# Optimization experiments

Measured on AMD Instinct MI355X. Metric: run time of the kernel, lower is better.

## Reference

```python
import jax, jax.numpy as jnp
import numpy as np

IN_SIZE = 1024
HIDDEN = 50
OUT_DIM = 8
BATCH = 16384
BN_EPS = 1e-5


def _gf(h, W1, b1, W2, b2):
    # graph_fusion: Linear -> LeakyReLU(0.2) -> Linear -> Tanh
    t = h @ W1 + b1
    t = jnp.where(t > 0, t, 0.2 * t)
    return jnp.tanh(t @ W2 + b2)


def _lrelu(z):
    return jnp.where(z > 0, z, 0.01 * z)  # F.leaky_relu default slope


def _dot(p, q):
    return jnp.sum(p * q, axis=-1)  # batched [B,1,D]@[B,D,1] -> [B]


def setup_inputs() -> dict:
    key = jax.random.key(0)
    ks = jax.random.split(key, 16)
    d, h, o = IN_SIZE, HIDDEN, OUT_DIM
    s = lambda n: 1.0 / np.sqrt(n)
    return {
        "x": jax.random.normal(ks[0], (BATCH, 3, d), jnp.float32),
        "att_W": jax.random.normal(ks[1], (d, 1), jnp.float32) * s(d),
        "att_b": jnp.zeros((1,), jnp.float32),
        "gf_W1": jax.random.normal(ks[2], (2 * d, 64), jnp.float32) * s(2 * d),
        "gf_b1": jnp.zeros((64,), jnp.float32),
        "gf_W2": jax.random.normal(ks[3], (64, d), jnp.float32) * s(64),
        "gf_b2": jnp.zeros((d,), jnp.float32),
        "bn_gamma": jnp.ones((3 * d,), jnp.float32),
        "bn_beta": jnp.zeros((3 * d,), jnp.float32),
        "l1_W": jax.random.normal(ks[4], (3 * d, h), jnp.float32) * s(3 * d),
        "l1_b": jnp.zeros((h,), jnp.float32),
        "l2_W": jax.random.normal(ks[5], (h, h), jnp.float32) * s(h),
        "l2_b": jnp.zeros((h,), jnp.float32),
        "l3_W": jax.random.normal(ks[6], (h, o), jnp.float32) * s(h),
        "l3_b": jnp.zeros((o,), jnp.float32),
    }


def _forward(x, att_W, att_b, gf_W1, gf_b1, gf_W2, gf_b2,
             bn_gamma, bn_beta, l1_W, l1_b, l2_W, l2_b, l3_W, l3_b):
    a1, v1, l1_ = x[:, 0, :], x[:, 1, :], x[:, 2, :]
    gf = lambda p, q: _gf(jnp.concatenate([p, q], axis=1), gf_W1, gf_b1, gf_W2, gf_b2)

    # unimodal attention weights, softmax over the 3 modalities
    att = jnp.tanh(x @ att_W + att_b)[..., 0]          # [B,3]
    w_uni = jax.nn.softmax(att, axis=1)                # [B,3]
    sa, sv, sl = w_uni[:, 0], w_uni[:, 1], w_uni[:, 2]
    unimodal = (sa[:, None] * a1 + sv[:, None] * v1 + sl[:, None] * l1_) / 3.0

    a = jax.nn.softmax(a1, axis=1)
    v = jax.nn.softmax(v1, axis=1)
    l = jax.nn.softmax(l1_, axis=1)
    sav = (sa + sv) / (_dot(a, v) + 0.5)
    sal = (sa + sl) / (_dot(a, l) + 0.5)
    svl = (sl + sv) / (_dot(v, l) + 0.5)
    w_bi = jax.nn.softmax(jnp.stack([sav, sal, svl], axis=1), axis=1)  # [B,3]

    a_v = _lrelu(w_bi[:, 0:1] * gf(a1, v1))
    a_l = _lrelu(w_bi[:, 1:2] * gf(a1, l1_))
    v_l = _lrelu(w_bi[:, 2:3] * gf(v1, l1_))
    bimodal = (a_v + a_l + v_l) / 3.0

    a_v2 = jax.nn.softmax(a_v, axis=1)
    a_l2 = jax.nn.softmax(a_l, axis=1)
    v_l2 = jax.nn.softmax(v_l, axis=1)
    savvl = (sav + svl) / (_dot(a_v2, v_l2) + 0.5)
    saavl = (sav + sal) / (_dot(a_v2, a_l2) + 0.5)
    savll = (sal + svl) / (_dot(a_l2, v_l2) + 0.5)
    savl = (sav + sl) / (_dot(a_v2, l) + 0.5)
    salv = (sal + sv) / (_dot(a_l2, v) + 0.5)
    svla = (sa + svl) / (_dot(v_l2, a) + 0.5)
    w_tri = jax.nn.softmax(
        jnp.stack([savvl, saavl, savll, savl, salv, svla], axis=1), axis=1)  # [B,6]

    avvl = _lrelu(w_tri[:, 0:1] * gf(a_v, v_l))
    aavl = _lrelu(w_tri[:, 1:2] * gf(a_v, a_l))
    avll = _lrelu(w_tri[:, 2:3] * gf(v_l, a_l))
    avl = _lrelu(w_tri[:, 3:4] * gf(a_v, l1_))
    alv = _lrelu(w_tri[:, 4:5] * gf(a_l, v1))
    vla = _lrelu(w_tri[:, 5:6] * gf(v_l, a1))
    trimodal = (avvl + aavl + avll + avl + alv + vla) / 6.0

    fusion = jnp.concatenate([unimodal, bimodal, trimodal], axis=1)  # [B,3*in]
    # BatchNorm1d in eval mode: running_mean=0, running_var=1
    fusion = fusion * (bn_gamma / jnp.sqrt(1.0 + BN_EPS)) + bn_beta
    y = jnp.tanh(fusion @ l1_W + l1_b)
    y = jnp.tanh(y @ l2_W + l2_b)
    y2 = jax.nn.softmax(y @ l3_W + l3_b, axis=1)
    total_weights = jnp.concatenate([w_uni, w_bi, w_tri], axis=1)  # [B,12]
    return y2, total_weights


def reference(x, att_W, att_b, gf_W1, gf_b1, gf_W2, gf_b2,
              bn_gamma, bn_beta, l1_W, l1_b, l2_W, l2_b, l3_W, l3_b):
    return _forward(x, att_W, att_b, gf_W1, gf_b1, gf_W2, gf_b2,
                    bn_gamma, bn_beta, l1_W, l1_b, l2_W, l2_b, l3_W, l3_b)
```

## Files before the change

### kernel.cpp

```cpp
#include <hip/hip_runtime.h>
#include <math.h>

#define NB 16384
#define DD 1024
#define KF 5120

typedef unsigned short u16;
typedef unsigned int u32;
typedef __attribute__((ext_vector_type(8))) short bf16x8;
typedef __attribute__((ext_vector_type(4))) float f32x4;

__device__ __forceinline__ float bf2f(u16 u){
  return __uint_as_float(((unsigned)u) << 16);
}
__device__ __forceinline__ u16 f2bf(float f){
  unsigned u = __float_as_uint(f);
  return (u16)((u + 0x7fffu + ((u >> 16) & 1u)) >> 16);
}
__device__ __forceinline__ u16 f2bf_tr(float f){
  return (u16)(__float_as_uint(f) >> 16);
}
__device__ __forceinline__ u32 pack2bf(float a, float b){
  return (u32)f2bf(a) | ((u32)f2bf(b) << 16);
}
__device__ __forceinline__ float fast_tanh(float x){
  float e = __expf(2.0f * x);
  return 1.0f - 2.0f * __builtin_amdgcn_rcpf(e + 1.0f);
}
__device__ __forceinline__ float wredsum(float x){
  #pragma unroll
  for(int o = 32; o >= 1; o >>= 1) x += __shfl_xor(x, o);
  return x;
}
__device__ __forceinline__ float wredmax(float x){
  #pragma unroll
  for(int o = 32; o >= 1; o >>= 1) x = fmaxf(x, __shfl_xor(x, o));
  return x;
}
__device__ __forceinline__ void gll16(const void* g, void* l){
  __builtin_amdgcn_global_load_lds(
      (const __attribute__((address_space(1))) u32*)g,
      (__attribute__((address_space(3))) u32*)l, 16, 0, 0);
}

__global__ __launch_bounds__(256) void kpre(
    const float* __restrict__ W1, const float* __restrict__ W2,
    const float* __restrict__ gamma, const float* __restrict__ beta,
    const float* __restrict__ l1W, const float* __restrict__ l1b,
    u16* __restrict__ Wb1, u16* __restrict__ W2T, u16* __restrict__ WpT,
    float* __restrict__ bp)
{
  __shared__ float red[4][64];
  int b = blockIdx.x, tid = threadIdx.x;
  if(b < 512){
    int idx = b*256 + tid;
    int n = idx >> 10, k = idx & 1023;
    float v = (n < 64) ? W1[(size_t)k*64 + n] : W1[(size_t)(1024+k)*64 + (n-64)];
    Wb1[idx] = f2bf(v);
  } else if(b < 768){
    int idx = (b-512)*256 + tid;
    int c = idx >> 6, k = idx & 63;
    W2T[idx] = f2bf(W2[(size_t)k*DD + c]);
  } else if(b < 2048){
    int idx = (b-768)*256 + tid;
    int j = idx / KF, kk = idx - j*KF;
    const float gsc = 1.0f / sqrtf(1.0f + 1e-5f);
    int korig; float sc;
    if(kk < 1024){ korig = kk; sc = 1.f; }
    else if(kk < 4096){ korig = 1024 + ((kk - 1024) & 1023); sc = 1.0f/3.0f; }
    else { korig = 2048 + (kk - 4096); sc = 1.f; }
    float v = (j < 50) ? l1W[(size_t)korig*50 + j] * gamma[korig] * gsc * sc : 0.f;
    WpT[(size_t)j*KF + kk] = f2bf(v);
  } else {
    int j = tid & 63, seg = tid >> 6;
    float s = 0.f;
    if(j < 50){
      for(int k = seg*768; k < seg*768 + 768; k++)
        s = fmaf(beta[k], l1W[(size_t)k*50 + j], s);
    }
    red[seg][j] = s;
    __syncthreads();
    if(seg == 0){
      float t = red[0][j] + red[1][j] + red[2][j] + red[3][j];
      bp[j] = (j < 50) ? (l1b[j] + t) : 0.f;
    }
  }
}

__global__ __launch_bounds__(256) void k1_stats(
    const float* __restrict__ x, const float* __restrict__ attW,
    const float* __restrict__ attb, float* __restrict__ stats,
    u16* __restrict__ uniB, u16* __restrict__ xb, float* __restrict__ tw)
{
  int wave = threadIdx.x >> 6, lane = threadIdx.x & 63;
  int r = blockIdx.x * 4 + wave;
  const float2* xr  = (const float2*)(x + (size_t)r * 3 * DD);
  const float2* aw2 = (const float2*)attW;
  float2 a[8], v[8], l[8];
  float dA=0.f,dV=0.f,dL=0.f, mA=-1e30f,mV=-1e30f,mL=-1e30f;
  #pragma unroll
  for(int i = 0; i < 8; i++){
    int k2 = lane + i*64;
    a[i] = xr[k2]; v[i] = xr[512+k2]; l[i] = xr[1024+k2];
    float2 w = aw2[k2];
    dA = fmaf(a[i].x, w.x, fmaf(a[i].y, w.y, dA));
    dV = fmaf(v[i].x, w.x, fmaf(v[i].y, w.y, dV));
    dL = fmaf(l[i].x, w.x, fmaf(l[i].y, w.y, dL));
    mA = fmaxf(mA, fmaxf(a[i].x, a[i].y));
    mV = fmaxf(mV, fmaxf(v[i].x, v[i].y));
    mL = fmaxf(mL, fmaxf(l[i].x, l[i].y));
  }
  dA = wredsum(dA); dV = wredsum(dV); dL = wredsum(dL);
  mA = wredmax(mA); mV = wredmax(mV); mL = wredmax(mL);

  u32* xbw = (u32*)(xb + (size_t)3*r*DD);
  #pragma unroll
  for(int i = 0; i < 8; i++){
    int k2 = lane + i*64;
    xbw[k2]      = pack2bf(a[i].x, a[i].y);
    xbw[512+k2]  = pack2bf(v[i].x, v[i].y);
    xbw[1024+k2] = pack2bf(l[i].x, l[i].y);
  }

  float Sa=0.f,Sv=0.f,Sl=0.f,Eav=0.f,Eal=0.f,Evl=0.f;
  #pragma unroll
  for(int i = 0; i < 8; i++){
    float eax = __expf(a[i].x-mA), eay = __expf(a[i].y-mA);
    float evx = __expf(v[i].x-mV), evy = __expf(v[i].y-mV);
    float elx = __expf(l[i].x-mL), ely = __expf(l[i].y-mL);
    Sa += eax+eay; Sv += evx+evy; Sl += elx+ely;
    Eav += eax*evx + eay*evy; Eal += eax*elx + eay*ely; Evl += evx*elx + evy*ely;
  }
  Sa = wredsum(Sa); Sv = wredsum(Sv); Sl = wredsum(Sl);
  Eav = wredsum(Eav); Eal = wredsum(Eal); Evl = wredsum(Evl);

  float ab = attb[0];
  float ta = fast_tanh(dA + ab), tv = fast_tanh(dV + ab), tl = fast_tanh(dL + ab);
  float mm = fmaxf(ta, fmaxf(tv, tl));
  float e0 = __expf(ta-mm), e1 = __expf(tv-mm), e2 = __expf(tl-mm);
  float ss = e0 + e1 + e2;
  float sa = e0/ss, sv = e1/ss, sl = e2/ss;
  float dav = Eav/(Sa*Sv), dal = Eal/(Sa*Sl), dvl = Evl/(Sv*Sl);
  float sav = (sa+sv)/(dav+0.5f);
  float sal = (sa+sl)/(dal+0.5f);
  float svl = (sv+sl)/(dvl+0.5f);
  float m2 = fmaxf(sav, fmaxf(sal, svl));
  float f0 = __expf(sav-m2), f1 = __expf(sal-m2), f2 = __expf(svl-m2);
  float s2 = f0 + f1 + f2;
  float wb0 = f0/s2, wb1 = f1/s2, wb2 = f2/s2;

  if(lane == 0){
    float* st = stats + (size_t)r*24;
    st[0]=sa; st[1]=sv; st[2]=sl;
    st[3]=wb0; st[4]=wb1; st[5]=wb2;
    st[6]=sav; st[7]=sal; st[8]=svl;
    st[9]=mA; st[10]=Sa; st[11]=mV; st[12]=Sv; st[13]=mL; st[14]=Sl;
    float* twr = tw + (size_t)r*12;
    twr[0]=sa; twr[1]=sv; twr[2]=sl; twr[3]=wb0; twr[4]=wb1; twr[5]=wb2;
  }
  u32* uniw = (u32*)(uniB + (size_t)r*DD);
  #pragma unroll
  for(int i = 0; i < 8; i++){
    int k2 = lane + i*64;
    float ux = (sa*a[i].x + sv*v[i].x + sl*l[i].x) * (1.0f/3.0f);
    float uy = (sa*a[i].y + sv*v[i].y + sl*l[i].y) * (1.0f/3.0f);
    uniw[k2] = pack2bf(ux, uy);
  }
}

__global__ __launch_bounds__(256) void kg1v3(
    const u16* __restrict__ src, const u16* __restrict__ Wb1,
    float* __restrict__ UV)
{
  __shared__ u16 Asm[2][64*64];
  int tid = threadIdx.x;
  int wv = tid >> 6, lane = tid & 63;
  int fr = lane & 15, kg = lane >> 4;
  int mb = blockIdx.x * 64;

  int r8 = lane >> 3, p = lane & 7;
  int sp = p ^ r8;
  int m0 = mb + (2*wv)*8 + r8;
  int m1 = mb + (2*wv+1)*8 + r8;
  const u16* gsrc0 = src + (size_t)m0*1024 + sp*8;
  const u16* gsrc1 = src + (size_t)m1*1024 + sp*8;

  f32x4 acc[4][2];
  #pragma unroll
  for(int rf = 0; rf < 4; rf++)
    #pragma unroll
    for(int nf = 0; nf < 2; nf++) acc[rf][nf] = (f32x4){0.f,0.f,0.f,0.f};

  gll16(gsrc0, &Asm[0][(2*wv)*512]);
  gll16(gsrc1, &Asm[0][(2*wv+1)*512]);
  __syncthreads();

  int buf = 0;
  for(int ci = 0; ci < 16; ci++){
    int k0 = ci*64;
    if(ci < 15){
      gll16(gsrc0 + k0 + 64, &Asm[buf^1][(2*wv)*512]);
      gll16(gsrc1 + k0 + 64, &Asm[buf^1][(2*wv+1)*512]);
    }
    #pragma unroll
    for(int ks = 0; ks < 2; ks++){
      bf16x8 a[4];
      #pragma unroll
      for(int rf = 0; rf < 4; rf++){
        int row = rf*16 + fr;
        int slot = (ks*4 + kg) ^ (row & 7);
        a[rf] = *(const bf16x8*)&Asm[buf][row*64 + slot*8];
      }
      #pragma unroll
      for(int nf = 0; nf < 2; nf++){
        int col = wv*32 + nf*16 + fr;
        bf16x8 b = *(const bf16x8*)&Wb1[(size_t)col*1024 + k0 + ks*32 + kg*8];
        #pragma unroll
        for(int rf = 0; rf < 4; rf++)
          acc[rf][nf] = __builtin_amdgcn_mfma_f32_16x16x32_bf16(a[rf], b, acc[rf][nf], 0, 0, 0);
      }
    }
    __syncthreads();
    buf ^= 1;
  }

  #pragma unroll
  for(int rf = 0; rf < 4; rf++)
    #pragma unroll
    for(int nf = 0; nf < 2; nf++)
      #pragma unroll
      for(int q = 0; q < 4; q++)
        UV[(size_t)(mb + rf*16 + kg*4 + q)*128 + wv*32 + nf*16 + fr] = acc[rf][nf][q];
}

__global__ __launch_bounds__(256) void kBI(
    const float* __restrict__ UV1, const u16* __restrict__ xb,
    const u16* __restrict__ W2T, const u16* __restrict__ Wb1,
    const u16* __restrict__ WpT, const float* __restrict__ b1,
    const float* __restrict__ b2, float* __restrict__ stats,
    float* __restrict__ tw, float* __restrict__ UV2, float* __restrict__ y1g)
{
  __shared__ u16 Tsm[3][16][64];
  __shared__ u16 Osm[4][16][264];
  __shared__ float stro[16][15];
  int tid = threadIdx.x;
  int wv = tid >> 6, lane = tid & 63;
  int fr = lane & 15, kg = lane >> 4;
  int Rb = blockIdx.x * 16;

  if(tid < 240){
    int r = tid / 15, c = tid - r*15;
    stro[r][c] = stats[(size_t)(Rb + r)*24 + c];
  }
  for(int i = tid; i < 384; i += 256){
    int g = i & 7, r = (i >> 3) & 15, p = i >> 7;
    int R = Rb + r;
    int up = (p == 2) ? 1 : 0;
    int vp = (p == 0) ? 1 : 2;
    const float* Up = UV1 + (size_t)(3*R + up)*128 + g*8;
    const float* Vp = UV1 + (size_t)(3*R + vp)*128 + 64 + g*8;
    float4 u0 = *(const float4*)Up, u1 = *(const float4*)(Up+4);
    float4 v0 = *(const float4*)Vp, v1 = *(const float4*)(Vp+4);
    float4 bb0 = *(const float4*)(b1 + g*8), bb1 = *(const float4*)(b1 + g*8 + 4);
    float t[8] = {u0.x+v0.x+bb0.x, u0.y+v0.y+bb0.y, u0.z+v0.z+bb0.z, u0.w+v0.w+bb0.w,
                  u1.x+v1.x+bb1.x, u1.y+v1.y+bb1.y, u1.z+v1.z+bb1.z, u1.w+v1.w+bb1.w};
    bf16x8 o;
    #pragma unroll
    for(int j = 0; j < 8; j++){
      float tv = t[j] > 0.f ? t[j] : 0.2f*t[j];
      o[j] = (short)f2bf_tr(tv);
    }
    *(bf16x8*)&Tsm[p][r][(g ^ (r & 7))*8] = o;
  }
  __syncthreads();

  f32x4 acc_uv[3][2];
  #pragma unroll
  for(int p = 0; p < 3; p++){ acc_uv[p][0] = (f32x4){0,0,0,0}; acc_uv[p][1] = (f32x4){0,0,0,0}; }
  f32x4 accy = (f32x4){0,0,0,0};
  int srow = tid >> 4, sc0 = (tid & 15) * 16;
  float SP[9] = {0,0,0,0,0,0,0,0,0};
  float mAr = stro[srow][9],  Sar = stro[srow][10];
  float mVr = stro[srow][11], Svr = stro[srow][12];
  float mLr = stro[srow][13], Slr = stro[srow][14];
  size_t xbase = (size_t)3*(Rb + srow)*DD;

  for(int cg = 0; cg < 4; cg++){
    f32x4 acc[3][4];
    #pragma unroll
    for(int p = 0; p < 3; p++)
      #pragma unroll
      for(int cf = 0; cf < 4; cf++) acc[p][cf] = (f32x4){0,0,0,0};
    #pragma unroll
    for(int ks = 0; ks < 2; ks++){
      bf16x8 a[3];
      #pragma unroll
      for(int p = 0; p < 3; p++)
        a[p] = *(const bf16x8*)&Tsm[p][fr][(((ks<<2)+kg) ^ (fr & 7))*8];
      #pragma unroll
      for(int cf = 0; cf < 4; cf++){
        bf16x8 b = *(const bf16x8*)&W2T[(size_t)(cg*256 + wv*64 + cf*16 + fr)*64
                                        + ks*32 + kg*8];
        #pragma unroll
        for(int p = 0; p < 3; p++)
          acc[p][cf] = __builtin_amdgcn_mfma_f32_16x16x32_bf16(a[p], b, acc[p][cf], 0, 0, 0);
      }
    }
    __syncthreads();
    #pragma unroll
    for(int q = 0; q < 4; q++){
      int row = kg*4 + q;
      #pragma unroll
      for(int cf = 0; cf < 4; cf++){
        int cloc = wv*64 + cf*16 + fr;
        float b2c = b2[cg*256 + cloc];
        float sm = 0.f;
        #pragma unroll
        for(int p = 0; p < 3; p++){
          float g = stro[row][3+p] * fast_tanh(acc[p][cf][q] + b2c);
          float val = g > 0.f ? g : 0.01f*g;
          Osm[p][row][cloc] = f2bf(val);
          sm += val;
        }
        Osm[3][row][cloc] = f2bf_tr(sm);
      }
    }
    __syncthreads();

    {
      const u32* xa1 = (const u32*)(xb + xbase + cg*256 + sc0);
      const u32* xv1 = (const u32*)(xb + xbase + DD + cg*256 + sc0);
      const u32* xl1 = (const u32*)(xb + xbase + 2*DD + cg*256 + sc0);
      #pragma unroll
      for(int j = 0; j < 8; j++){
        u32 oav = *(const u32*)&Osm[0][srow][sc0 + 2*j];
        u32 oal = *(const u32*)&Osm[1][srow][sc0 + 2*j];
        u32 ovl = *(const u32*)&Osm[2][srow][sc0 + 2*j];
        u32 wa = xa1[j], wvv = xv1[j], wl = xl1[j];
        float eavx = __expf(bf2f((u16)oav)), eavy = __expf(bf2f((u16)(oav>>16)));
        float ealx = __expf(bf2f((u16)oal)), ealy = __expf(bf2f((u16)(oal>>16)));
        float evlx = __expf(bf2f((u16)ovl)), evly = __expf(bf2f((u16)(ovl>>16)));
        float eax = __expf(bf2f((u16)wa)-mAr),  eay = __expf(bf2f((u16)(wa>>16))-mAr);
        float evx = __expf(bf2f((u16)wvv)-mVr), evy = __expf(bf2f((u16)(wvv>>16))-mVr);
        float elx = __expf(bf2f((u16)wl)-mLr),  ely = __expf(bf2f((u16)(wl>>16))-mLr);
        SP[0] += eavx+eavy; SP[1] += ealx+ealy; SP[2] += evlx+evly;
        SP[3] += eavx*evlx + eavy*evly;
        SP[4] += eavx*ealx + eavy*ealy;
        SP[5] += ealx*evlx + ealy*evly;
        SP[6] += eavx*elx + eavy*ely;
        SP[7] += ealx*evx + ealy*evy;
        SP[8] += evlx*eax + evly*eay;
      }
    }
    #pragma unroll
    for(int ks8 = 0; ks8 < 8; ks8++){
      bf16x8 a[3];
      #pragma unroll
      for(int p = 0; p < 3; p++)
        a[p] = *(const bf16x8*)&Osm[p][fr][ks8*32 + kg*8];
      #pragma unroll
      for(int nf = 0; nf < 2; nf++){
        int n = wv*32 + nf*16 + fr;
        bf16x8 b = *(const bf16x8*)&Wb1[(size_t)n*1024 + cg*256 + ks8*32 + kg*8];
        #pragma unroll
        for(int p = 0; p < 3; p++)
          acc_uv[p][nf] = __builtin_amdgcn_mfma_f32_16x16x32_bf16(a[p], b, acc_uv[p][nf], 0, 0, 0);
      }
    }
    #pragma unroll
    for(int kq = 0; kq < 4; kq++)
      #pragma unroll
      for(int ks = 0; ks < 2; ks++){
        bf16x8 a = *(const bf16x8*)&Osm[3][fr][kq*64 + ks*32 + kg*8];
        bf16x8 b = *(const bf16x8*)&WpT[(size_t)(wv*16 + fr)*KF + 1024 + cg*256
                                        + kq*64 + ks*32 + kg*8];
        accy = __builtin_amdgcn_mfma_f32_16x16x32_bf16(a, b, accy, 0, 0, 0);
      }
  }

  #pragma unroll
  for(int p = 0; p < 3; p++)
    #pragma unroll
    for(int nf = 0; nf < 2; nf++)
      #pragma unroll
      for(int q = 0; q < 4; q++)
        UV2[(size_t)(3*(Rb + kg*4 + q) + p)*128 + wv*32 + nf*16 + fr] = acc_uv[p][nf][q];
  #pragma unroll
  for(int q = 0; q < 4; q++)
    y1g[(size_t)(Rb + kg*4 + q)*64 + wv*16 + fr] = accy[q];

  #pragma unroll
  for(int s = 0; s < 9; s++){
    SP[s] += __shfl_xor(SP[s], 1);
    SP[s] += __shfl_xor(SP[s], 2);
    SP[s] += __shfl_xor(SP[s], 4);
    SP[s] += __shfl_xor(SP[s], 8);
  }
  if((tid & 15) == 0){
    int r = srow;
    float sa=stro[r][0], sv=stro[r][1], sl=stro[r][2];
    float sav=stro[r][6], sal=stro[r][7], svl=stro[r][8];
    float d1 = SP[3]/(SP[0]*SP[2]), d2 = SP[4]/(SP[0]*SP[1]), d3 = SP[5]/(SP[1]*SP[2]);
    float d4 = SP[6]/(SP[0]*Slr),   d5 = SP[7]/(SP[1]*Svr),   d6 = SP[8]/(SP[2]*Sar);
    float t0 = (sav+svl)/(d1+0.5f);
    float t1 = (sav+sal)/(d2+0.5f);
    float t2 = (sal+svl)/(d3+0.5f);
    float t3 = (sav+sl)/(d4+0.5f);
    float t4 = (sal+sv)/(d5+0.5f);
    float t5 = (sa+svl)/(d6+0.5f);
    float mx = fmaxf(fmaxf(fmaxf(t0,t1),fmaxf(t2,t3)),fmaxf(t4,t5));
    float g0=__expf(t0-mx),g1=__expf(t1-mx),g2=__expf(t2-mx);
    float g3=__expf(t3-mx),g4=__expf(t4-mx),g5=__expf(t5-mx);
    float gs = g0+g1+g2+g3+g4+g5;
    float wt[6] = {g0/gs,g1/gs,g2/gs,g3/gs,g4/gs,g5/gs};
    float* st = stats + (size_t)(Rb + r)*24;
    float* twr = tw + (size_t)(Rb + r)*12;
    #pragma unroll
    for(int p = 0; p < 6; p++){ st[15+p] = wt[p]; twr[6+p] = wt[p]; }
  }
}

__global__ __launch_bounds__(256) void kTRI(
    const float* __restrict__ UV2, const float* __restrict__ UV1,
    const u16* __restrict__ W2T, const u16* __restrict__ WpT,
    const float* __restrict__ b1, const float* __restrict__ b2,
    const float* __restrict__ stats, float* __restrict__ y1g)
{
  __shared__ u16 Tsm[6][16][64];
  __shared__ u16 Osm[16][264];
  __shared__ float stw[16][6];
  int tid = threadIdx.x;
  int wv = tid >> 6, lane = tid & 63;
  int fr = lane & 15, kg = lane >> 4;
  int Rb = blockIdx.x * 16;

  if(tid < 96){
    int r = tid / 6, p = tid - r*6;
    stw[r][p] = stats[(size_t)(Rb + r)*24 + 15 + p];
  }
  for(int i = tid; i < 768; i += 256){
    int g = i & 7, r = (i >> 3) & 15, p = i >> 7;
    int R = Rb + r;
    int up = (0x210200 >> (p*4)) & 15;
    int vp = (0x012112 >> (p*4)) & 15;
    const float* VB = (p < 3) ? UV2 : UV1;
    const float* Up = UV2 + (size_t)(3*R + up)*128 + g*8;
    const float* Vp = VB  + (size_t)(3*R + vp)*128 + 64 + g*8;
    float4 u0 = *(const float4*)Up, u1 = *(const float4*)(Up+4);
    float4 v0 = *(const float4*)Vp, v1 = *(const float4*)(Vp+4);
    float4 bb0 = *(const float4*)(b1 + g*8), bb1 = *(const float4*)(b1 + g*8 + 4);
    float t[8] = {u0.x+v0.x+bb0.x, u0.y+v0.y+bb0.y, u0.z+v0.z+bb0.z, u0.w+v0.w+bb0.w,
                  u1.x+v1.x+bb1.x, u1.y+v1.y+bb1.y, u1.z+v1.z+bb1.z, u1.w+v1.w+bb1.w};
    bf16x8 o;
    #pragma unroll
    for(int j = 0; j < 8; j++){
      float tv = t[j] > 0.f ? t[j] : 0.2f*t[j];
      o[j] = (short)f2bf_tr(tv);
    }
    *(bf16x8*)&Tsm[p][r][(g ^ (r & 7))*8] = o;
  }
  __syncthreads();

  f32x4 accy = (f32x4){0,0,0,0};
  for(int cg = 0; cg < 4; cg++){
    f32x4 acc[6][4];
    #pragma unroll
    for(int p = 0; p < 6; p++)
      #pragma unroll
      for(int cf = 0; cf < 4; cf++) acc[p][cf] = (f32x4){0,0,0,0};
    #pragma unroll
    for(int ks = 0; ks < 2; ks++){
      bf16x8 a[6];
      #pragma unroll
      for(int p = 0; p < 6; p++)
        a[p] = *(const bf16x8*)&Tsm[p][fr][(((ks<<2)+kg) ^ (fr & 7))*8];
      #pragma unroll
      for(int cf = 0; cf < 4; cf++){
        bf16x8 b = *(const bf16x8*)&W2T[(size_t)(cg*256 + wv*64 + cf*16 + fr)*64
                                        + ks*32 + kg*8];
        #pragma unroll
        for(int p = 0; p < 6; p++)
          acc[p][cf] = __builtin_amdgcn_mfma_f32_16x16x32_bf16(a[p], b, acc[p][cf], 0, 0, 0);
      }
    }
    __syncthreads();
    #pragma unroll
    for(int q = 0; q < 4; q++){
      int row = kg*4 + q;
      #pragma unroll
      for(int cf = 0; cf < 4; cf++){
        int cloc = wv*64 + cf*16 + fr;
        float b2c = b2[cg*256 + cloc];
        float s = 0.f;
        #pragma unroll
        for(int p = 0; p < 6; p++){
          float g = stw[row][p] * fast_tanh(acc[p][cf][q] + b2c);
          s += g > 0.f ? g : 0.01f*g;
        }
        Osm[row][cloc] = f2bf_tr(s * (1.0f/6.0f));
      }
    }
    __syncthreads();
    #pragma unroll
    for(int kq = 0; kq < 4; kq++)
      #pragma unroll
      for(int ks = 0; ks < 2; ks++){
        bf16x8 a = *(const bf16x8*)&Osm[fr][kq*64 + ks*32 + kg*8];
        bf16x8 b = *(const bf16x8*)&WpT[(size_t)(wv*16 + fr)*KF + 4096 + cg*256
                                        + kq*64 + ks*32 + kg*8];
        accy = __builtin_amdgcn_mfma_f32_16x16x32_bf16(a, b, accy, 0, 0, 0);
      }
  }
  #pragma unroll
  for(int q = 0; q < 4; q++){
    size_t idx = (size_t)(Rb + kg*4 + q)*64 + wv*16 + fr;
    y1g[idx] += accy[q];
  }
}

__global__ __launch_bounds__(256) void k6v5(
    const u16* __restrict__ uniB, const u16* __restrict__ WpT,
    const float* __restrict__ y1g, const float* __restrict__ bp,
    const float* __restrict__ l2W, const float* __restrict__ l2b,
    const float* __restrict__ l3W, const float* __restrict__ l3b,
    float* __restrict__ y2out)
{
  __shared__ __align__(16) char smem[37952];
  u16*  Asm = (u16*)smem;
  float* W2s = (float*)(smem + 16384);
  float* W3s = (float*)(smem + 16384 + 12800);
  float* Ys  = (float*)smem;
  float* Ys2 = (float*)(smem + 16384 + 12800 + 1600);

  int tid = threadIdx.x;
  int wv = tid >> 6, lane = tid & 63;
  int fr = lane & 15, kg = lane >> 4;
  int rb = blockIdx.x * 32;

  for(int t = tid; t < 3200; t += 256){
    int c = t & 63;
    W2s[t] = (c < 50) ? l2W[(t >> 6)*50 + c] : 0.f;
  }
  for(int t = tid; t < 400; t += 256) W3s[t] = l3W[t];

  int r8 = lane >> 3, pp = lane & 7;
  int sp = pp ^ r8;
  const u16* gsrc = uniB + (size_t)(rb + wv*8 + r8)*DD + sp*8;
  const u16* bptr = WpT  + (size_t)(wv*16 + fr)*KF + kg*8;

  f32x4 acc[2];
  acc[0] = (f32x4){0.f,0.f,0.f,0.f};
  acc[1] = (f32x4){0.f,0.f,0.f,0.f};

  gll16(gsrc,      &Asm[wv*1024]);
  gll16(gsrc + 64, &Asm[wv*1024 + 512]);
  __syncthreads();

  int buf = 0;
  for(int ci = 0; ci < 8; ci++){
    int k0 = ci*128;
    if(ci < 7){
      gll16(gsrc + k0 + 128, &Asm[(buf^1)*4096 + wv*1024]);
      gll16(gsrc + k0 + 192, &Asm[(buf^1)*4096 + wv*1024 + 512]);
    }
    #pragma unroll
    for(int kh = 0; kh < 2; kh++){
      #pragma unroll
      for(int ks = 0; ks < 2; ks++){
        bf16x8 b = *(const bf16x8*)(bptr + k0 + kh*64 + ks*32);
        #pragma unroll
        for(int rf = 0; rf < 2; rf++){
          int row = rf*16 + fr;
          int slot = ((ks<<2) + kg) ^ (row & 7);
          bf16x8 a = *(const bf16x8*)&Asm[buf*4096 + (row>>3)*1024 + kh*512
                                          + (row & 7)*64 + slot*8];
          acc[rf] = __builtin_amdgcn_mfma_f32_16x16x32_bf16(a, b, acc[rf], 0, 0, 0);
        }
      }
    }
    __syncthreads();
    buf ^= 1;
  }

  {
    int col = wv*16 + fr;
    float bpc = bp[col];
    #pragma unroll
    for(int rf = 0; rf < 2; rf++)
      #pragma unroll
      for(int q = 0; q < 4; q++){
        int row = rf*16 + kg*4 + q;
        if(col < 50){
          float z = acc[rf][q] + y1g[(size_t)(rb + row)*64 + col] + bpc;
          Ys[row*56 + col] = fast_tanh(z);
        }
      }
  }
  __syncthreads();

  {
    int r = tid >> 3, cg = (tid & 7) * 7;
    float a2[7] = {0,0,0,0,0,0,0};
    for(int k = 0; k < 50; k++){
      float yv = Ys[r*56 + k];
      #pragma unroll
      for(int c = 0; c < 7; c++) a2[c] = fmaf(yv, W2s[k*64 + cg + c], a2[c]);
    }
    #pragma unroll
    for(int c = 0; c < 7; c++){
      int cc = cg + c;
      if(cc < 50) Ys2[r*56 + cc] = fast_tanh(a2[c] + l2b[cc]);
    }
  }
  __syncthreads();

  {
    int r = tid >> 3, c = tid & 7;
    float z = l3b[c];
    for(int k = 0; k < 50; k++) z = fmaf(Ys2[r*56 + k], W3s[k*8 + c], z);
    float m = z;
    m = fmaxf(m, __shfl_xor(m, 1));
    m = fmaxf(m, __shfl_xor(m, 2));
    m = fmaxf(m, __shfl_xor(m, 4));
    float e = __expf(z - m);
    float s = e;
    s += __shfl_xor(s, 1); s += __shfl_xor(s, 2); s += __shfl_xor(s, 4);
    y2out[(size_t)(rb + r)*8 + c] = e / s;
  }
}

extern "C" void kernel_launch(void* const* d_in, const int* in_sizes, int n_in,
                              void* d_out, int out_size, void* d_ws, size_t ws_size,
                              hipStream_t stream)
{
  (void)in_sizes; (void)n_in; (void)out_size; (void)ws_size;
  const float* x    = (const float*)d_in[0];
  const float* attW = (const float*)d_in[1];
  const float* attb = (const float*)d_in[2];
  const float* gfW1 = (const float*)d_in[3];
  const float* gfb1 = (const float*)d_in[4];
  const float* gfW2 = (const float*)d_in[5];
  const float* gfb2 = (const float*)d_in[6];
  const float* bng  = (const float*)d_in[7];
  const float* bnb  = (const float*)d_in[8];
  const float* l1W  = (const float*)d_in[9];
  const float* l1b  = (const float*)d_in[10];
  const float* l2W  = (const float*)d_in[11];
  const float* l2b  = (const float*)d_in[12];
  const float* l3W  = (const float*)d_in[13];
  const float* l3b  = (const float*)d_in[14];

  float* out = (float*)d_out;
  float* tw  = out + (size_t)NB*8;

  float* ws    = (float*)d_ws;
  float* stats = ws;
  float* UV1   = stats + (size_t)NB*24;
  float* UV2   = UV1 + (size_t)3*NB*128;
  float* bp    = UV2 + (size_t)3*NB*128;
  float* y1g   = bp + 64;
  u16* WpT     = (u16*)(y1g + (size_t)NB*64);
  u16* Wb1     = WpT + (size_t)64*KF;
  u16* W2T     = Wb1 + (size_t)128*1024;
  u16* xb      = W2T + (size_t)1024*64;
  u16* uniB    = xb + (size_t)3*NB*DD;

  kpre<<<dim3(2049), dim3(256), 0, stream>>>(gfW1, gfW2, bng, bnb, l1W, l1b,
                                             Wb1, W2T, WpT, bp);
  k1_stats<<<dim3(NB/4), dim3(256), 0, stream>>>(x, attW, attb, stats, uniB, xb, tw);
  kg1v3<<<dim3(3*NB/64), dim3(256), 0, stream>>>(xb, Wb1, UV1);
  kBI<<<dim3(NB/16), dim3(256), 0, stream>>>(UV1, xb, W2T, Wb1, WpT,
                                             gfb1, gfb2, stats, tw, UV2, y1g);
  kTRI<<<dim3(NB/16), dim3(256), 0, stream>>>(UV2, UV1, W2T, WpT,
                                              gfb1, gfb2, stats, y1g);
  k6v5<<<dim3(NB/32), dim3(256), 0, stream>>>(uniB, WpT, y1g, bp,
                                              l2W, l2b, l3W, l3b, out);
}
```

Measured before the change: 449.9 us.

## Split bimodal/trimodal stages across column slabs with atomics and separate GEMM pass

The bimodal and trimodal kernels now run on a 2D grid with one block per (16-row group, 256-column slab) instead of looping over four column groups serially. Partial y1 contributions and softmax statistics are accumulated with atomicAdd into buffers that the prep kernel zeroes. The bimodal outputs are written to a bf16 Fcat buffer, and a templated reuse of the first-layer GEMM kernel computes UV2 from it instead of fusing that GEMM into the bimodal kernel. k1_stats also moves to float4 loads and uint2 stores. This raises parallelism and occupancy, at the cost of extra global traffic for Fcat, an additional kernel launch and atomic contention.

After: 379.9 us. 1.18x faster.

```diff
diff --git a/kernel.cpp b/kernel.cpp
--- a/kernel.cpp
+++ b/kernel.cpp
@@ -48,7 +48,7 @@
     const float* __restrict__ gamma, const float* __restrict__ beta,
     const float* __restrict__ l1W, const float* __restrict__ l1b,
     u16* __restrict__ Wb1, u16* __restrict__ W2T, u16* __restrict__ WpT,
-    float* __restrict__ bp)
+    float* __restrict__ bp, float* __restrict__ y1g, float* __restrict__ spart)
 {
   __shared__ float red[4][64];
   int b = blockIdx.x, tid = threadIdx.x;
@@ -71,6 +71,12 @@
     else { korig = 2048 + (kk - 4096); sc = 1.f; }
     float v = (j < 50) ? l1W[(size_t)korig*50 + j] * gamma[korig] * gsc * sc : 0.f;
     WpT[(size_t)j*KF + kk] = f2bf(v);
+  } else if(b < 3072){
+    int idx = (b - 2048)*256 + tid;
+    ((float4*)y1g)[idx] = make_float4(0.f,0.f,0.f,0.f);
+  } else if(b < 3216){
+    int idx = (b - 3072)*256 + tid;
+    ((float4*)spart)[idx] = make_float4(0.f,0.f,0.f,0.f);
   } else {
     int j = tid & 63, seg = tid >> 6;
     float s = 0.f;
@@ -94,42 +100,44 @@
 {
   int wave = threadIdx.x >> 6, lane = threadIdx.x & 63;
   int r = blockIdx.x * 4 + wave;
-  const float2* xr  = (const float2*)(x + (size_t)r * 3 * DD);
-  const float2* aw2 = (const float2*)attW;
-  float2 a[8], v[8], l[8];
+  const float4* xr  = (const float4*)(x + (size_t)r * 3 * DD);
+  const float4* aw4 = (const float4*)attW;
+  float4 a[4], v[4], l[4];
   float dA=0.f,dV=0.f,dL=0.f, mA=-1e30f,mV=-1e30f,mL=-1e30f;
   #pragma unroll
-  for(int i = 0; i < 8; i++){
-    int k2 = lane + i*64;
-    a[i] = xr[k2]; v[i] = xr[512+k2]; l[i] = xr[1024+k2];
-    float2 w = aw2[k2];
-    dA = fmaf(a[i].x, w.x, fmaf(a[i].y, w.y, dA));
-    dV = fmaf(v[i].x, w.x, fmaf(v[i].y, w.y, dV));
-    dL = fmaf(l[i].x, w.x, fmaf(l[i].y, w.y, dL));
-    mA = fmaxf(mA, fmaxf(a[i].x, a[i].y));
-    mV = fmaxf(mV, fmaxf(v[i].x, v[i].y));
-    mL = fmaxf(mL, fmaxf(l[i].x, l[i].y));
+  for(int i = 0; i < 4; i++){
+    int k4 = lane + i*64;
+    a[i] = xr[k4]; v[i] = xr[256+k4]; l[i] = xr[512+k4];
+    float4 w = aw4[k4];
+    dA = fmaf(a[i].x,w.x, fmaf(a[i].y,w.y, fmaf(a[i].z,w.z, fmaf(a[i].w,w.w, dA))));
+    dV = fmaf(v[i].x,w.x, fmaf(v[i].y,w.y, fmaf(v[i].z,w.z, fmaf(v[i].w,w.w, dV))));
+    dL = fmaf(l[i].x,w.x, fmaf(l[i].y,w.y, fmaf(l[i].z,w.z, fmaf(l[i].w,w.w, dL))));
+    mA = fmaxf(mA, fmaxf(fmaxf(a[i].x,a[i].y), fmaxf(a[i].z,a[i].w)));
+    mV = fmaxf(mV, fmaxf(fmaxf(v[i].x,v[i].y), fmaxf(v[i].z,v[i].w)));
+    mL = fmaxf(mL, fmaxf(fmaxf(l[i].x,l[i].y), fmaxf(l[i].z,l[i].w)));
   }
   dA = wredsum(dA); dV = wredsum(dV); dL = wredsum(dL);
   mA = wredmax(mA); mV = wredmax(mV); mL = wredmax(mL);
 
-  u32* xbw = (u32*)(xb + (size_t)3*r*DD);
-  #pragma unroll
-  for(int i = 0; i < 8; i++){
-    int k2 = lane + i*64;
-    xbw[k2]      = pack2bf(a[i].x, a[i].y);
-    xbw[512+k2]  = pack2bf(v[i].x, v[i].y);
-    xbw[1024+k2] = pack2bf(l[i].x, l[i].y);
+  uint2* xbw = (uint2*)(xb + (size_t)3*r*DD);
+  #pragma unroll
+  for(int i = 0; i < 4; i++){
+    int k4 = lane + i*64;
+    xbw[k4]     = make_uint2(pack2bf(a[i].x,a[i].y), pack2bf(a[i].z,a[i].w));
+    xbw[256+k4] = make_uint2(pack2bf(v[i].x,v[i].y), pack2bf(v[i].z,v[i].w));
+    xbw[512+k4] = make_uint2(pack2bf(l[i].x,l[i].y), pack2bf(l[i].z,l[i].w));
   }
 
   float Sa=0.f,Sv=0.f,Sl=0.f,Eav=0.f,Eal=0.f,Evl=0.f;
   #pragma unroll
-  for(int i = 0; i < 8; i++){
-    float eax = __expf(a[i].x-mA), eay = __expf(a[i].y-mA);
-    float evx = __expf(v[i].x-mV), evy = __expf(v[i].y-mV);
-    float elx = __expf(l[i].x-mL), ely = __expf(l[i].y-mL);
-    Sa += eax+eay; Sv += evx+evy; Sl += elx+ely;
-    Eav += eax*evx + eay*evy; Eal += eax*elx + eay*ely; Evl += evx*elx + evy*ely;
+  for(int i = 0; i < 4; i++){
+    float ea0=__expf(a[i].x-mA), ea1=__expf(a[i].y-mA), ea2=__expf(a[i].z-mA), ea3=__expf(a[i].w-mA);
+    float ev0=__expf(v[i].x-mV), ev1=__expf(v[i].y-mV), ev2=__expf(v[i].z-mV), ev3=__expf(v[i].w-mV);
+    float el0=__expf(l[i].x-mL), el1=__expf(l[i].y-mL), el2=__expf(l[i].z-mL), el3=__expf(l[i].w-mL);
+    Sa += ea0+ea1+ea2+ea3; Sv += ev0+ev1+ev2+ev3; Sl += el0+el1+el2+el3;
+    Eav += ea0*ev0 + ea1*ev1 + ea2*ev2 + ea3*ev3;
+    Eal += ea0*el0 + ea1*el1 + ea2*el2 + ea3*el3;
+    Evl += ev0*el0 + ev1*el1 + ev2*el2 + ev3*el3;
   }
   Sa = wredsum(Sa); Sv = wredsum(Sv); Sl = wredsum(Sl);
   Eav = wredsum(Eav); Eal = wredsum(Eal); Evl = wredsum(Evl);
@@ -158,16 +166,19 @@
     float* twr = tw + (size_t)r*12;
     twr[0]=sa; twr[1]=sv; twr[2]=sl; twr[3]=wb0; twr[4]=wb1; twr[5]=wb2;
   }
-  u32* uniw = (u32*)(uniB + (size_t)r*DD);
-  #pragma unroll
-  for(int i = 0; i < 8; i++){
-    int k2 = lane + i*64;
-    float ux = (sa*a[i].x + sv*v[i].x + sl*l[i].x) * (1.0f/3.0f);
-    float uy = (sa*a[i].y + sv*v[i].y + sl*l[i].y) * (1.0f/3.0f);
-    uniw[k2] = pack2bf(ux, uy);
-  }
-}
-
+  uint2* uniw = (uint2*)(uniB + (size_t)r*DD);
+  #pragma unroll
+  for(int i = 0; i < 4; i++){
+    int k4 = lane + i*64;
+    float u0 = (sa*a[i].x + sv*v[i].x + sl*l[i].x) * (1.0f/3.0f);
+    float u1 = (sa*a[i].y + sv*v[i].y + sl*l[i].y) * (1.0f/3.0f);
+    float u2 = (sa*a[i].z + sv*v[i].z + sl*l[i].z) * (1.0f/3.0f);
+    float u3 = (sa*a[i].w + sv*v[i].w + sl*l[i].w) * (1.0f/3.0f);
+    uniw[k4] = make_uint2(pack2bf(u0,u1), pack2bf(u2,u3));
+  }
+}
+
+template<int FCAT>
 __global__ __launch_bounds__(256) void kg1v3(
     const u16* __restrict__ src, const u16* __restrict__ Wb1,
     float* __restrict__ UV)
@@ -182,8 +193,17 @@
   int sp = p ^ r8;
   int m0 = mb + (2*wv)*8 + r8;
   int m1 = mb + (2*wv+1)*8 + r8;
-  const u16* gsrc0 = src + (size_t)m0*1024 + sp*8;
-  const u16* gsrc1 = src + (size_t)m1*1024 + sp*8;
+  size_t b0, b1;
+  if(FCAT){
+    int R0 = m0/3, R1 = m1/3;
+    b0 = (size_t)R0*KF + (size_t)(1 + (m0 - 3*R0))*1024;
+    b1 = (size_t)R1*KF + (size_t)(1 + (m1 - 3*R1))*1024;
+  } else {
+    b0 = (size_t)m0*1024;
+    b1 = (size_t)m1*1024;
+  }
+  const u16* gsrc0 = src + b0 + sp*8;
+  const u16* gsrc1 = src + b1 + sp*8;
 
   f32x4 acc[4][2];
   #pragma unroll
@@ -233,12 +253,12 @@
         UV[(size_t)(mb + rf*16 + kg*4 + q)*128 + wv*32 + nf*16 + fr] = acc[rf][nf][q];
 }
 
-__global__ __launch_bounds__(256) void kBI(
+__global__ __launch_bounds__(256) void kL2bi(
     const float* __restrict__ UV1, const u16* __restrict__ xb,
-    const u16* __restrict__ W2T, const u16* __restrict__ Wb1,
-    const u16* __restrict__ WpT, const float* __restrict__ b1,
-    const float* __restrict__ b2, float* __restrict__ stats,
-    float* __restrict__ tw, float* __restrict__ UV2, float* __restrict__ y1g)
+    const u16* __restrict__ W2T, const u16* __restrict__ WpT,
+    const float* __restrict__ b1, const float* __restrict__ b2,
+    const float* __restrict__ stats, u16* __restrict__ Fcat,
+    float* __restrict__ y1g, float* __restrict__ spart)
 {
   __shared__ u16 Tsm[3][16][64];
   __shared__ u16 Osm[4][16][264];
@@ -247,10 +267,11 @@
   int wv = tid >> 6, lane = tid & 63;
   int fr = lane & 15, kg = lane >> 4;
   int Rb = blockIdx.x * 16;
+  int slab = blockIdx.y;
 
   if(tid < 240){
-    int r = tid / 15, c = tid - r*15;
-    stro[r][c] = stats[(size_t)(Rb + r)*24 + c];
+    int rr = tid / 15, c = tid - rr*15;
+    stro[rr][c] = stats[(size_t)(Rb + rr)*24 + c];
   }
   for(int i = tid; i < 384; i += 256){
     int g = i & 7, r = (i >> 3) & 15, p = i >> 7;
@@ -274,134 +295,144 @@
   }
   __syncthreads();
 
-  f32x4 acc_uv[3][2];
-  #pragma unroll
-  for(int p = 0; p < 3; p++){ acc_uv[p][0] = (f32x4){0,0,0,0}; acc_uv[p][1] = (f32x4){0,0,0,0}; }
-  f32x4 accy = (f32x4){0,0,0,0};
-  int srow = tid >> 4, sc0 = (tid & 15) * 16;
-  float SP[9] = {0,0,0,0,0,0,0,0,0};
-  float mAr = stro[srow][9],  Sar = stro[srow][10];
-  float mVr = stro[srow][11], Svr = stro[srow][12];
-  float mLr = stro[srow][13], Slr = stro[srow][14];
-  size_t xbase = (size_t)3*(Rb + srow)*DD;
-
-  for(int cg = 0; cg < 4; cg++){
-    f32x4 acc[3][4];
+  f32x4 acc[3][4];
+  #pragma unroll
+  for(int p = 0; p < 3; p++)
+    #pragma unroll
+    for(int cf = 0; cf < 4; cf++) acc[p][cf] = (f32x4){0,0,0,0};
+  #pragma unroll
+  for(int ks = 0; ks < 2; ks++){
+    bf16x8 a[3];
     #pragma unroll
     for(int p = 0; p < 3; p++)
-      #pragma unroll
-      for(int cf = 0; cf < 4; cf++) acc[p][cf] = (f32x4){0,0,0,0};
-    #pragma unroll
-    for(int ks = 0; ks < 2; ks++){
-      bf16x8 a[3];
+      a[p] = *(const bf16x8*)&Tsm[p][fr][(((ks<<2)+kg) ^ (fr & 7))*8];
+    #pragma unroll
+    for(int cf = 0; cf < 4; cf++){
+      bf16x8 b = *(const bf16x8*)&W2T[(size_t)(slab*256 + wv*64 + cf*16 + fr)*64
+                                      + ks*32 + kg*8];
       #pragma unroll
       for(int p = 0; p < 3; p++)
-        a[p] = *(const bf16x8*)&Tsm[p][fr][(((ks<<2)+kg) ^ (fr & 7))*8];
-      #pragma unroll
-      for(int cf = 0; cf < 4; cf++){
-        bf16x8 b = *(const bf16x8*)&W2T[(size_t)(cg*256 + wv*64 + cf*16 + fr)*64
-                                        + ks*32 + kg*8];
-        #pragma unroll
-        for(int p = 0; p < 3; p++)
-          acc[p][cf] = __builtin_amdgcn_mfma_f32_16x16x32_bf16(a[p], b, acc[p][cf], 0, 0, 0);
-      }
-    }
-    __syncthreads();
-    #pragma unroll
-    for(int q = 0; q < 4; q++){
-      int row = kg*4 + q;
-      #pragma unroll
-      for(int cf = 0; cf < 4; cf++){
-        int cloc = wv*64 + cf*16 + fr;
-        float b2c = b2[cg*256 + cloc];
-        float sm = 0.f;
-        #pragma unroll
-        for(int p = 0; p < 3; p++){
-          float g = stro[row][3+p] * fast_tanh(acc[p][cf][q] + b2c);
-          float val = g > 0.f ? g : 0.01f*g;
-          Osm[p][row][cloc] = f2bf(val);
-          sm += val;
-        }
-        Osm[3][row][cloc] = f2bf_tr(sm);
-      }
-    }
-    __syncthreads();
-
-    {
-      const u32* xa1 = (const u32*)(xb + xbase + cg*256 + sc0);
-      const u32* xv1 = (const u32*)(xb + xbase + DD + cg*256 + sc0);
-      const u32* xl1 = (const u32*)(xb + xbase + 2*DD + cg*256 + sc0);
-      #pragma unroll
-      for(int j = 0; j < 8; j++){
-        u32 oav = *(const u32*)&Osm[0][srow][sc0 + 2*j];
-        u32 oal = *(const u32*)&Osm[1][srow][sc0 + 2*j];
-        u32 ovl = *(const u32*)&Osm[2][srow][sc0 + 2*j];
-        u32 wa = xa1[j], wvv = xv1[j], wl = xl1[j];
-        float eavx = __expf(bf2f((u16)oav)), eavy = __expf(bf2f((u16)(oav>>16)));
-        float ealx = __expf(bf2f((u16)oal)), ealy = __expf(bf2f((u16)(oal>>16)));
-        float evlx = __expf(bf2f((u16)ovl)), evly = __expf(bf2f((u16)(ovl>>16)));
-        float eax = __expf(bf2f((u16)wa)-mAr),  eay = __expf(bf2f((u16)(wa>>16))-mAr);
-        float evx = __expf(bf2f((u16)wvv)-mVr), evy = __expf(bf2f((u16)(wvv>>16))-mVr);
-        float elx = __expf(bf2f((u16)wl)-mLr),  ely = __expf(bf2f((u16)(wl>>16))-mLr);
-        SP[0] += eavx+eavy; SP[1] += ealx+ealy; SP[2] += evlx+evly;
-        SP[3] += eavx*evlx + eavy*evly;
-        SP[4] += eavx*ealx + eavy*ealy;
-        SP[5] += ealx*evlx + ealy*evly;
-        SP[6] += eavx*elx + eavy*ely;
-        SP[7] += ealx*evx + ealy*evy;
-        SP[8] += evlx*eax + evly*eay;
-      }
-    }
-    #pragma unroll
-    for(int ks8 = 0; ks8 < 8; ks8++){
-      bf16x8 a[3];
-      #pragma unroll
-      for(int p = 0; p < 3; p++)
-        a[p] = *(const bf16x8*)&Osm[p][fr][ks8*32 + kg*8];
-      #pragma unroll
-      for(int nf = 0; nf < 2; nf++){
-        int n = wv*32 + nf*16 + fr;
-        bf16x8 b = *(const bf16x8*)&Wb1[(size_t)n*1024 + cg*256 + ks8*32 + kg*8];
-        #pragma unroll
-        for(int p = 0; p < 3; p++)
-          acc_uv[p][nf] = __builtin_amdgcn_mfma_f32_16x16x32_bf16(a[p], b, acc_uv[p][nf], 0, 0, 0);
-      }
-    }
+        acc[p][cf] = __builtin_amdgcn_mfma_f32_16x16x32_bf16(a[p], b, acc[p][cf], 0, 0, 0);
+    }
+  }
+
+  #pragma unroll
+  for(int q = 0; q < 4; q++){
+    int row = kg*4 + q;
+    #pragma unroll
+    for(int cf = 0; cf < 4; cf++){
+      int cloc = wv*64 + cf*16 + fr;
+      float b2c = b2[slab*256 + cloc];
+      float sm = 0.f;
+      #pragma unroll
+      for(int p = 0; p < 3; p++){
+        float g = stro[row][3+p] * fast_tanh(acc[p][cf][q] + b2c);
+        float val = g > 0.f ? g : 0.01f*g;
+        Osm[p][row][cloc] = f2bf(val);
+        sm += val;
+      }
+      Osm[3][row][cloc] = f2bf_tr(sm);
+    }
+  }
+  __syncthreads();
+
+  {
+    int orow = tid >> 4, oc16 = (tid & 15) * 16;
+    #pragma unroll
+    for(int p = 0; p < 3; p++){
+      bf16x8 o0 = *(const bf16x8*)&Osm[p][orow][oc16];
+      bf16x8 o1 = *(const bf16x8*)&Osm[p][orow][oc16 + 8];
+      size_t off = (size_t)(Rb + orow)*KF + (size_t)(1+p)*1024 + slab*256 + oc16;
+      *(bf16x8*)&Fcat[off]     = o0;
+      *(bf16x8*)&Fcat[off + 8] = o1;
+    }
+  }
+
+  {
+    const u16* bptr = WpT + (size_t)(wv*16 + fr)*KF + 1024 + slab*256 + kg*8;
+    f32x4 accy = (f32x4){0,0,0,0};
     #pragma unroll
     for(int kq = 0; kq < 4; kq++)
       #pragma unroll
       for(int ks = 0; ks < 2; ks++){
         bf16x8 a = *(const bf16x8*)&Osm[3][fr][kq*64 + ks*32 + kg*8];
-        bf16x8 b = *(const bf16x8*)&WpT[(size_t)(wv*16 + fr)*KF + 1024 + cg*256
-                                        + kq*64 + ks*32 + kg*8];
+        bf16x8 b = *(const bf16x8*)(bptr + kq*64 + ks*32);
         accy = __builtin_amdgcn_mfma_f32_16x16x32_bf16(a, b, accy, 0, 0, 0);
       }
-  }
-
-  #pragma unroll
-  for(int p = 0; p < 3; p++)
-    #pragma unroll
-    for(int nf = 0; nf < 2; nf++)
-      #pragma unroll
-      for(int q = 0; q < 4; q++)
-        UV2[(size_t)(3*(Rb + kg*4 + q) + p)*128 + wv*32 + nf*16 + fr] = acc_uv[p][nf][q];
-  #pragma unroll
-  for(int q = 0; q < 4; q++)
-    y1g[(size_t)(Rb + kg*4 + q)*64 + wv*16 + fr] = accy[q];
-
-  #pragma unroll
-  for(int s = 0; s < 9; s++){
-    SP[s] += __shfl_xor(SP[s], 1);
-    SP[s] += __shfl_xor(SP[s], 2);
-    SP[s] += __shfl_xor(SP[s], 4);
-    SP[s] += __shfl_xor(SP[s], 8);
-  }
-  if((tid & 15) == 0){
-    int r = srow;
-    float sa=stro[r][0], sv=stro[r][1], sl=stro[r][2];
-    float sav=stro[r][6], sal=stro[r][7], svl=stro[r][8];
-    float d1 = SP[3]/(SP[0]*SP[2]), d2 = SP[4]/(SP[0]*SP[1]), d3 = SP[5]/(SP[1]*SP[2]);
-    float d4 = SP[6]/(SP[0]*Slr),   d5 = SP[7]/(SP[1]*Svr),   d6 = SP[8]/(SP[2]*Sar);
+    #pragma unroll
+    for(int q = 0; q < 4; q++)
+      atomicAdd(&y1g[(size_t)(Rb + kg*4 + q)*64 + wv*16 + fr], accy[q]);
+  }
+
+  {
+    int srow = tid >> 4, sc0 = (tid & 15) * 16;
+    float mAr = stro[srow][9], mVr = stro[srow][11], mLr = stro[srow][13];
+    size_t xbase = (size_t)3*(Rb + srow)*DD + slab*256;
+    const u32* xa1 = (const u32*)(xb + xbase);
+    const u32* xv1 = (const u32*)(xb + xbase + DD);
+    const u32* xl1 = (const u32*)(xb + xbase + 2*DD);
+    float SP[9] = {0,0,0,0,0,0,0,0,0};
+    #pragma unroll
+    for(int j = 0; j < 8; j++){
+      u32 oav = *(const u32*)&Osm[0][srow][sc0 + 2*j];
+      u32 oal = *(const u32*)&Osm[1][srow][sc0 + 2*j];
+      u32 ovl = *(const u32*)&Osm[2][srow][sc0 + 2*j];
+      u32 wa = xa1[(sc0>>1)+j], wvv = xv1[(sc0>>1)+j], wl = xl1[(sc0>>1)+j];
+      float eavx = __expf(bf2f((u16)oav)), eavy = __expf(bf2f((u16)(oav>>16)));
+      float ealx = __expf(bf2f((u16)oal)), ealy = __expf(bf2f((u16)(oal>>16)));
+      float evlx = __expf(bf2f((u16)ovl)), evly = __expf(bf2f((u16)(ovl>>16)));
+      float eax = __expf(bf2f((u16)wa)-mAr),  eay = __expf(bf2f((u16)(wa>>16))-mAr);
+      float evx = __expf(bf2f((u16)wvv)-mVr), evy = __expf(bf2f((u16)(wvv>>16))-mVr);
+      float elx = __expf(bf2f((u16)wl)-mLr),  ely = __expf(bf2f((u16)(wl>>16))-mLr);
+      SP[0] += eavx+eavy; SP[1] += ealx+ealy; SP[2] += evlx+evly;
+      SP[3] += eavx*evlx + eavy*evly;
+      SP[4] += eavx*ealx + eavy*ealy;
+      SP[5] += ealx*evlx + ealy*evly;
+      SP[6] += eavx*elx + eavy*ely;
+      SP[7] += ealx*evx + ealy*evy;
+      SP[8] += evlx*eax + evly*eay;
+    }
+    #pragma unroll
+    for(int s = 0; s < 9; s++){
+      SP[s] += __shfl_xor(SP[s], 1);
+      SP[s] += __shfl_xor(SP[s], 2);
+      SP[s] += __shfl_xor(SP[s], 4);
+      SP[s] += __shfl_xor(SP[s], 8);
+    }
+    if((tid & 15) == 0){
+      float* spr = spart + (size_t)(Rb + srow)*9;
+      #pragma unroll
+      for(int s = 0; s < 9; s++) atomicAdd(&spr[s], SP[s]);
+    }
+  }
+}
+
+__global__ __launch_bounds__(256) void kTRIv2(
+    const float* __restrict__ UV2, const float* __restrict__ UV1,
+    const u16* __restrict__ W2T, const u16* __restrict__ WpT,
+    const float* __restrict__ b1, const float* __restrict__ b2,
+    const float* __restrict__ stats, const float* __restrict__ spart,
+    float* __restrict__ tw, float* __restrict__ y1g)
+{
+  __shared__ u16 Tsm[6][16][64];
+  __shared__ u16 Osm[16][264];
+  __shared__ float stw[16][6];
+  int tid = threadIdx.x;
+  int wv = tid >> 6, lane = tid & 63;
+  int fr = lane & 15, kg = lane >> 4;
+  int Rb = blockIdx.x * 16;
+  int slab = blockIdx.y;
+
+  if(tid < 16){
+    int R = Rb + tid;
+    const float* st = stats + (size_t)R*24;
+    const float* sp = spart + (size_t)R*9;
+    float sa=st[0], sv=st[1], sl=st[2];
+    float sav=st[6], sal=st[7], svl=st[8];
+    float Sa=st[10], Sv=st[12], Sl=st[14];
+    float s0=sp[0], s1=sp[1], s2=sp[2];
+    float d1 = sp[3]/(s0*s2), d2 = sp[4]/(s0*s1), d3 = sp[5]/(s1*s2);
+    float d4 = sp[6]/(s0*Sl), d5 = sp[7]/(s1*Sv), d6 = sp[8]/(s2*Sa);
     float t0 = (sav+svl)/(d1+0.5f);
     float t1 = (sav+sal)/(d2+0.5f);
     float t2 = (sal+svl)/(d3+0.5f);
@@ -413,30 +444,13 @@
     float g3=__expf(t3-mx),g4=__expf(t4-mx),g5=__expf(t5-mx);
     float gs = g0+g1+g2+g3+g4+g5;
     float wt[6] = {g0/gs,g1/gs,g2/gs,g3/gs,g4/gs,g5/gs};
-    float* st = stats + (size_t)(Rb + r)*24;
-    float* twr = tw + (size_t)(Rb + r)*12;
-    #pragma unroll
-    for(int p = 0; p < 6; p++){ st[15+p] = wt[p]; twr[6+p] = wt[p]; }
-  }
-}
-
-__global__ __launch_bounds__(256) void kTRI(
-    const float* __restrict__ UV2, const float* __restrict__ UV1,
-    const u16* __restrict__ W2T, const u16* __restrict__ WpT,
-    const float* __restrict__ b1, const float* __restrict__ b2,
-    const float* __restrict__ stats, float* __restrict__ y1g)
-{
-  __shared__ u16 Tsm[6][16][64];
-  __shared__ u16 Osm[16][264];
-  __shared__ float stw[16][6];
-  int tid = threadIdx.x;
-  int wv = tid >> 6, lane = tid & 63;
-  int fr = lane & 15, kg = lane >> 4;
-  int Rb = blockIdx.x * 16;
-
-  if(tid < 96){
-    int r = tid / 6, p = tid - r*6;
-    stw[r][p] = stats[(size_t)(Rb + r)*24 + 15 + p];
+    #pragma unroll
+    for(int p = 0; p < 6; p++) stw[tid][p] = wt[p];
+    if(slab == 0){
+      float* twr = tw + (size_t)R*12;
+      #pragma unroll
+      for(int p = 0; p < 6; p++) twr[6+p] = wt[p];
+    }
   }
   for(int i = tid; i < 768; i += 256){
     int g = i & 7, r = (i >> 3) & 15, p = i >> 7;
@@ -461,60 +475,59 @@
   }
   __syncthreads();
 
-  f32x4 accy = (f32x4){0,0,0,0};
-  for(int cg = 0; cg < 4; cg++){
-    f32x4 acc[6][4];
+  f32x4 acc[6][4];
+  #pragma unroll
+  for(int p = 0; p < 6; p++)
+    #pragma unroll
+    for(int cf = 0; cf < 4; cf++) acc[p][cf] = (f32x4){0,0,0,0};
+  #pragma unroll
+  for(int ks = 0; ks < 2; ks++){
+    bf16x8 a[6];
     #pragma unroll
     for(int p = 0; p < 6; p++)
-      #pragma unroll
-      for(int cf = 0; cf < 4; cf++) acc[p][cf] = (f32x4){0,0,0,0};
-    #pragma unroll
-    for(int ks = 0; ks < 2; ks++){
-      bf16x8 a[6];
+      a[p] = *(const bf16x8*)&Tsm[p][fr][(((ks<<2)+kg) ^ (fr & 7))*8];
+    #pragma unroll
+    for(int cf = 0; cf < 4; cf++){
+      bf16x8 b = *(const bf16x8*)&W2T[(size_t)(slab*256 + wv*64 + cf*16 + fr)*64
+                                      + ks*32 + kg*8];
       #pragma unroll
       for(int p = 0; p < 6; p++)
-        a[p] = *(const bf16x8*)&Tsm[p][fr][(((ks<<2)+kg) ^ (fr & 7))*8];
-      #pragma unroll
-      for(int cf = 0; cf < 4; cf++){
-        bf16x8 b = *(const bf16x8*)&W2T[(size_t)(cg*256 + wv*64 + cf*16 + fr)*64
-                                        + ks*32 + kg*8];
-        #pragma unroll
-        for(int p = 0; p < 6; p++)
-          acc[p][cf] = __builtin_amdgcn_mfma_f32_16x16x32_bf16(a[p], b, acc[p][cf], 0, 0, 0);
-      }
-    }
-    __syncthreads();
-    #pragma unroll
-    for(int q = 0; q < 4; q++){
-      int row = kg*4 + q;
-      #pragma unroll
-      for(int cf = 0; cf < 4; cf++){
-        int cloc = wv*64 + cf*16 + fr;
-        float b2c = b2[cg*256 + cloc];
-        float s = 0.f;
-        #pragma unroll
-        for(int p = 0; p < 6; p++){
-          float g = stw[row][p] * fast_tanh(acc[p][cf][q] + b2c);
-          s += g > 0.f ? g : 0.01f*g;
-        }
-        Osm[row][cloc] = f2bf_tr(s * (1.0f/6.0f));
-      }
-    }
-    __syncthreads();
+        acc[p][cf] = __builtin_amdgcn_mfma_f32_16x16x32_bf16(a[p], b, acc[p][cf], 0, 0, 0);
+    }
+  }
+
+  #pragma unroll
+  for(int q = 0; q < 4; q++){
+    int row = kg*4 + q;
+    #pragma unroll
+    for(int cf = 0; cf < 4; cf++){
+      int cloc = wv*64 + cf*16 + fr;
+      float b2c = b2[slab*256 + cloc];
+      float s = 0.f;
+      #pragma unroll
+      for(int p = 0; p < 6; p++){
+        float g = stw[row][p] * fast_tanh(acc[p][cf][q] + b2c);
+        s += g > 0.f ? g : 0.01f*g;
+      }
+      Osm[row][cloc] = f2bf_tr(s * (1.0f/6.0f));
+    }
+  }
+  __syncthreads();
+
+  {
+    const u16* bptr = WpT + (size_t)(wv*16 + fr)*KF + 4096 + slab*256 + kg*8;
+    f32x4 accy = (f32x4){0,0,0,0};
     #pragma unroll
     for(int kq = 0; kq < 4; kq++)
       #pragma unroll
       for(int ks = 0; ks < 2; ks++){
         bf16x8 a = *(const bf16x8*)&Osm[fr][kq*64 + ks*32 + kg*8];
-        bf16x8 b = *(const bf16x8*)&WpT[(size_t)(wv*16 + fr)*KF + 4096 + cg*256
-                                        + kq*64 + ks*32 + kg*8];
+        bf16x8 b = *(const bf16x8*)(bptr + kq*64 + ks*32);
         accy = __builtin_amdgcn_mfma_f32_16x16x32_bf16(a, b, accy, 0, 0, 0);
       }
-  }
-  #pragma unroll
-  for(int q = 0; q < 4; q++){
-    size_t idx = (size_t)(Rb + kg*4 + q)*64 + wv*16 + fr;
-    y1g[idx] += accy[q];
+    #pragma unroll
+    for(int q = 0; q < 4; q++)
+      atomicAdd(&y1g[(size_t)(Rb + kg*4 + q)*64 + wv*16 + fr], accy[q]);
   }
 }
 
@@ -659,20 +672,23 @@
   float* UV2   = UV1 + (size_t)3*NB*128;
   float* bp    = UV2 + (size_t)3*NB*128;
   float* y1g   = bp + 64;
-  u16* WpT     = (u16*)(y1g + (size_t)NB*64);
+  float* spart = y1g + (size_t)NB*64;
+  u16* WpT     = (u16*)(spart + (size_t)NB*9);
   u16* Wb1     = WpT + (size_t)64*KF;
   u16* W2T     = Wb1 + (size_t)128*1024;
-  u16* xb      = W2T + (size_t)1024*64;
+  u16* Fcat    = W2T + (size_t)1024*64;
+  u16* xb      = Fcat + (size_t)NB*KF;
   u16* uniB    = xb + (size_t)3*NB*DD;
 
-  kpre<<<dim3(2049), dim3(256), 0, stream>>>(gfW1, gfW2, bng, bnb, l1W, l1b,
-                                             Wb1, W2T, WpT, bp);
+  kpre<<<dim3(3217), dim3(256), 0, stream>>>(gfW1, gfW2, bng, bnb, l1W, l1b,
+                                             Wb1, W2T, WpT, bp, y1g, spart);
   k1_stats<<<dim3(NB/4), dim3(256), 0, stream>>>(x, attW, attb, stats, uniB, xb, tw);
-  kg1v3<<<dim3(3*NB/64), dim3(256), 0, stream>>>(xb, Wb1, UV1);
-  kBI<<<dim3(NB/16), dim3(256), 0, stream>>>(UV1, xb, W2T, Wb1, WpT,
-                                             gfb1, gfb2, stats, tw, UV2, y1g);
-  kTRI<<<dim3(NB/16), dim3(256), 0, stream>>>(UV2, UV1, W2T, WpT,
-                                              gfb1, gfb2, stats, y1g);
+  kg1v3<0><<<dim3(3*NB/64), dim3(256), 0, stream>>>(xb, Wb1, UV1);
+  kL2bi<<<dim3(NB/16, 4), dim3(256), 0, stream>>>(UV1, xb, W2T, WpT,
+                                                  gfb1, gfb2, stats, Fcat, y1g, spart);
+  kg1v3<1><<<dim3(3*NB/64), dim3(256), 0, stream>>>(Fcat, Wb1, UV2);
+  kTRIv2<<<dim3(NB/16, 4), dim3(256), 0, stream>>>(UV2, UV1, W2T, WpT,
+                                                   gfb1, gfb2, stats, spart, tw, y1g);
   k6v5<<<dim3(NB/32), dim3(256), 0, stream>>>(uniB, WpT, y1g, bp,
                                               l2W, l2b, l3W, l3b, out);
 }
```
